# Kernel optimization log

Measured on AMD Instinct MI355X. Metric: run time of the kernel, lower is better.

## Reference

```python
import jax, jax.numpy as jnp
import numpy as np

B, N1, N2, D, O = 4, 256, 256, 64, 64
TEMP = 1.0
BN_EPS = 1e-5


def setup_inputs() -> dict:
    key = jax.random.key(0)
    ks = jax.random.split(key, 24)
    s = lambda n: 1.0 / np.sqrt(n)
    inp = {
        'x1': jax.random.normal(ks[0], (B, N1, D), jnp.float32),
        'x2': jax.random.normal(ks[1], (B, N2, D), jnp.float32),
        'W_t1': jax.random.normal(ks[2], (D, D), jnp.float32) * s(D),
        'b_t1': jnp.zeros((D,), jnp.float32),
        'W_t2': jax.random.normal(ks[3], (D, D), jnp.float32) * s(D),
        'b_t2': jnp.zeros((D,), jnp.float32),
        'W_att': jax.random.normal(ks[4], (D, O), jnp.float32) * s(D),
        'b_att': jnp.zeros((O,), jnp.float32),
        'W_attM': jax.random.normal(ks[5], (D, O), jnp.float32) * s(D),
        'b_attM': jnp.zeros((O,), jnp.float32),
        'w11': jax.random.normal(ks[6], (O, 1), jnp.float32) * s(O),
        'w22': jax.random.normal(ks[7], (O, 1), jnp.float32) * s(O),
        'w12': jax.random.normal(ks[8], (O, 1), jnp.float32) * s(O),
        'wM': jax.random.normal(ks[9], (O, 1), jnp.float32) * s(O),
        'W_pa': jax.random.normal(ks[10], (D, O), jnp.float32) * s(D),
        'b_pa': jnp.zeros((O,), jnp.float32),
        'W_po': jax.random.normal(ks[11], (D, O), jnp.float32) * s(D),
        'b_po': jnp.zeros((O,), jnp.float32),
        'W_paM': jax.random.normal(ks[12], (D, O), jnp.float32) * s(D),
        'b_paM': jnp.zeros((O,), jnp.float32),
        'W_poM': jax.random.normal(ks[13], (D, O), jnp.float32) * s(D),
        'b_poM': jnp.zeros((O,), jnp.float32),
        'gamma': jnp.ones((O,), jnp.float32),
        'beta': jnp.zeros((O,), jnp.float32),
    }
    return inp


def _forward(x1, x2, W_t1, b_t1, W_t2, b_t2, W_att, b_att, W_attM, b_attM,
             w11, w22, w12, wM, W_pa, b_pa, W_po, b_po, W_paM, b_paM,
             W_poM, b_poM, gamma, beta):
    n1 = x1.shape[1]
    h1 = x1 @ W_t1 + b_t1                      # (B,n1,D)
    h2 = x2 @ W_t2 + b_t2                      # (B,n2,D)
    x = jnp.concatenate([h1, h2], axis=1)      # (B,N,D)
    master = jnp.mean(x, axis=1, keepdims=True)  # (B,1,D)

    # --- type-blocked attention map ---
    pair = x[:, :, None, :] * x[:, None, :, :]          # (B,N,N,D)
    e = jnp.tanh(pair @ W_att + b_att)                   # (B,N,N,O)
    s11 = jnp.einsum('bijd,d->bij', e[:, :n1, :n1], w11[:, 0])
    s12 = jnp.einsum('bijd,d->bij', e[:, :n1, n1:], w12[:, 0])
    s21 = jnp.einsum('bijd,d->bij', e[:, n1:, :n1], w12[:, 0])
    s22 = jnp.einsum('bijd,d->bij', e[:, n1:, n1:], w22[:, 0])
    top = jnp.concatenate([s11, s12], axis=2)
    bot = jnp.concatenate([s21, s22], axis=2)
    scores = jnp.concatenate([top, bot], axis=1)         # (B,N,N)
    att = jax.nn.softmax(scores / TEMP, axis=2)          # softmax over source nodes (torch dim=-2 of (B,N,N,1))

    # --- master update ---
    m = jnp.tanh((x * master) @ W_attM + b_attM)         # (B,N,O)
    aM = jax.nn.softmax((m @ wM) / TEMP, axis=1)         # (B,N,1)
    agg_m = jnp.einsum('bn,bnd->bd', aM[:, :, 0], x)[:, None, :]  # (B,1,D)
    master_new = (agg_m @ W_paM + b_paM) + (master @ W_poM + b_poM)

    # --- node projection + BN(eval) + SELU ---
    agg = jnp.einsum('bij,bjd->bid', att, x)             # (B,N,D)
    y = (agg @ W_pa + b_pa) + (x @ W_po + b_po)          # (B,N,O)
    y = y / jnp.sqrt(1.0 + BN_EPS) * gamma + beta        # BN eval: mean=0, var=1
    y = jax.nn.selu(y)
    return y[:, :n1], y[:, n1:], master_new


def reference(x1, x2, W_t1, b_t1, W_t2, b_t2, W_att, b_att, W_attM, b_attM,
              w11, w22, w12, wM, W_pa, b_pa, W_po, b_po, W_paM, b_paM,
              W_poM, b_poM, gamma, beta):
    return _forward(x1, x2, W_t1, b_t1, W_t2, b_t2, W_att, b_att, W_attM,
                    b_attM, w11, w22, w12, wM, W_pa, b_pa, W_po, b_po,
                    W_paM, b_paM, W_poM, b_poM, gamma, beta)
```

## Files before the change

kernel.cpp:

```cpp
#include <hip/hip_runtime.h>

#define BB 4
#define NN 512
#define NH 256
#define DD 64

typedef __attribute__((ext_vector_type(8))) short bf16x8;
typedef __attribute__((ext_vector_type(16))) float f32x16;
union BF8 { bf16x8 v; unsigned int u[4]; };
union BF8Q { bf16x8 v; uint4 q; };

__device__ __forceinline__ float wred_sum(float v) {
  v += __shfl_xor(v, 32);
  v += __shfl_xor(v, 16);
  v += __shfl_xor(v, 8);
  v += __shfl_xor(v, 4);
  v += __shfl_xor(v, 2);
  v += __shfl_xor(v, 1);
  return v;
}

__device__ __forceinline__ float wred_max(float v) {
  v = fmaxf(v, __shfl_xor(v, 32));
  v = fmaxf(v, __shfl_xor(v, 16));
  v = fmaxf(v, __shfl_xor(v, 8));
  v = fmaxf(v, __shfl_xor(v, 4));
  v = fmaxf(v, __shfl_xor(v, 2));
  v = fmaxf(v, __shfl_xor(v, 1));
  return v;
}

__device__ __forceinline__ unsigned int cvtpk_bf16(float lo, float hi) {
  unsigned int r;
  asm("v_cvt_pk_bf16_f32 %0, %1, %2" : "=v"(r) : "v"(lo), "v"(hi));
  return r;
}

__device__ __forceinline__ float fast_exp2(float x) {
  float r;
  asm("v_exp_f32 %0, %1" : "=v"(r) : "v"(x));
  return r;
}

__device__ __forceinline__ float fast_tanh(float t) {
  t = fminf(15.f, fmaxf(-15.f, t));
  float z = __expf(2.f * t);
  return 1.f - 2.f * __builtin_amdgcn_rcpf(z + 1.f);
}

__device__ __forceinline__ float bflo(unsigned int u) { return __uint_as_float(u << 16); }
__device__ __forceinline__ float bfhi(unsigned int u) { return __uint_as_float(u & 0xffff0000u); }

__global__ __launch_bounds__(256)
void k1_build_x(const float* __restrict__ x1, const float* __restrict__ x2,
                const float* __restrict__ W_t1, const float* __restrict__ b_t1,
                const float* __restrict__ W_t2, const float* __restrict__ b_t2,
                float* __restrict__ X, unsigned int* __restrict__ XbfG) {
  const int tid = threadIdx.x;
  const int lane = tid & 63;
  const int rq = tid >> 6;
  const int r = blockIdx.x * 4 + rq;
  const int b = r >> 9;
  const int n = r & 511;
  const float* src; const float* W; const float* bias;
  if (n < NH) { src = x1 + (b * NH + n) * DD;        W = W_t1; bias = b_t1; }
  else        { src = x2 + (b * NH + (n - NH)) * DD; W = W_t2; bias = b_t2; }
  const float4* s4 = reinterpret_cast<const float4*>(src);
  float t0 = 0.f, t1 = 0.f, t2 = 0.f, t3 = 0.f;
#pragma unroll
  for (int c = 0; c < 16; ++c) {
    const float4 v = s4[c];
    t0 = fmaf(v.x, W[(4 * c + 0) * DD + lane], t0);
    t1 = fmaf(v.y, W[(4 * c + 1) * DD + lane], t1);
    t2 = fmaf(v.z, W[(4 * c + 2) * DD + lane], t2);
    t3 = fmaf(v.w, W[(4 * c + 3) * DD + lane], t3);
  }
  const float yv = ((t0 + t1) + (t2 + t3)) + bias[lane];
  X[r * DD + lane] = yv;
  const float nb = __shfl_down(yv, 1);
  if ((lane & 1) == 0) XbfG[r * 32 + (lane >> 1)] = cvtpk_bf16(yv, nb);
}

__global__ __launch_bounds__(512, 1)
void k_sc(const unsigned int* __restrict__ Xbf,
          const float* __restrict__ W_att, const float* __restrict__ b_att,
          const float* __restrict__ w11, const float* __restrict__ w22,
          const float* __restrict__ w12,
          float* __restrict__ scG) {
  const int b = blockIdx.y;
  const int bx = blockIdx.x;
  const int tid = threadIdx.x;
  const int lane = tid & 63;
  const int w = tid >> 6;
  const int l31 = lane & 31;
  const int half = lane >> 5;

  __shared__ __align__(16) float tblB[64];
  __shared__ __align__(16) unsigned int A2L[4][32];

  const unsigned int* __restrict__ Xb = Xbf + b * NN * 32;
  float* __restrict__ scb = scG + b * NN * NN;
  const float K2E = 2.8853900817779268f;

  if (tid < 64) {
    const int ot = tid >> 5, hf = (tid >> 4) & 1, r = tid & 15;
    const int o = ot * 32 + (r & 3) + 8 * (r >> 2) + 4 * hf;
    tblB[tid] = K2E * b_att[o];
  }
  if (tid >= 64 && tid < 320) {
    const int tt = tid - 64;
    const int comb = tt >> 6;
    const int idx = tt & 63;
    if (idx < 32) {
      const int ot = (idx >> 4) & 1, kg = (idx >> 3) & 1, hf = (idx >> 2) & 1, pp = idx & 3;
      const int it_ = comb >> 1, jt_ = comb & 1;
      const float* wsl = it_ ? (jt_ ? w22 : w12) : (jt_ ? w12 : w11);
      const int e0 = 2 * pp, e1 = 2 * pp + 1;
      const int o0 = ot * 32 + kg * 16 + (e0 & 3) + 8 * (e0 >> 2) + 4 * hf;
      const int o1 = ot * 32 + kg * 16 + (e1 & 3) + 8 * (e1 >> 2) + 4 * hf;
      A2L[comb][idx] = cvtpk_bf16(wsl[o0], wsl[o1]);
    }
  }

  BF8 Wp[2][4];
#pragma unroll
  for (int ot = 0; ot < 2; ++ot)
#pragma unroll
    for (int kt = 0; kt < 4; ++kt) {
      const int o = ot * 32 + l31;
#pragma unroll
      for (int pp = 0; pp < 4; ++pp) {
        const int d0 = kt * 16 + half * 8 + 2 * pp;
        Wp[ot][kt].u[pp] = cvtpk_bf16(W_att[d0 * DD + o], W_att[(d0 + 1) * DD + o]);
      }
    }

  __syncthreads();

  const int cminA = bx >> 4;
  const int n32A = 16 - cminA;
  const int rB = 510 - 2 * bx;
  const int cminB = (255 - bx) >> 4;
  const int njobs = 2 * (n32A + (16 - cminB));

#pragma unroll 1
  for (int jb = w; jb < njobs; jb += 8) {
    int row, c32;
    if (jb < 2 * n32A) { row = 2 * bx + (jb & 1); c32 = cminA + (jb >> 1); }
    else { const int tp = jb - 2 * n32A; row = rB + (tp & 1); c32 = cminB + (tp >> 1); }
    const int j0 = c32 * 32;
    const int comb = ((row >= NH) ? 2 : 0) | ((j0 >= NH) ? 1 : 0);

    BF8 Bi[4];
#pragma unroll
    for (int kt = 0; kt < 4; ++kt) {
      const uint4 xi = *reinterpret_cast<const uint4*>(Xb + row * 32 + kt * 8 + half * 4);
      const uint4 xj = *reinterpret_cast<const uint4*>(Xb + (j0 + l31) * 32 + kt * 8 + half * 4);
      Bi[kt].u[0] = cvtpk_bf16(bflo(xi.x) * bflo(xj.x), bfhi(xi.x) * bfhi(xj.x));
      Bi[kt].u[1] = cvtpk_bf16(bflo(xi.y) * bflo(xj.y), bfhi(xi.y) * bfhi(xj.y));
      Bi[kt].u[2] = cvtpk_bf16(bflo(xi.z) * bflo(xj.z), bfhi(xi.z) * bfhi(xj.z));
      Bi[kt].u[3] = cvtpk_bf16(bflo(xi.w) * bflo(xj.w), bfhi(xi.w) * bfhi(xj.w));
    }

    f32x16 C0 = {}, C1 = {};
#pragma unroll
    for (int kt = 0; kt < 4; ++kt) {
      C0 = __builtin_amdgcn_mfma_f32_32x32x16_bf16(Wp[0][kt].v, Bi[kt].v, C0, 0, 0, 0);
      C1 = __builtin_amdgcn_mfma_f32_32x32x16_bf16(Wp[1][kt].v, Bi[kt].v, C1, 0, 0, 0);
    }

    f32x16 D2 = {};
    const int base = half * 16;
#pragma unroll
    for (int ot = 0; ot < 2; ++ot) {
      float tv[16];
#pragma unroll
      for (int r = 0; r < 16; ++r) {
        const float Cr = (ot == 0) ? C0[r] : C1[r];
        const float arg = fmaf(Cr, K2E, tblB[ot * 32 + base + r]);
        const float e = fast_exp2(arg);
        tv[r] = fmaf(-2.f, __builtin_amdgcn_rcpf(e + 1.f), 1.f);
      }
      BF8 B2a, B2b;
#pragma unroll
      for (int pp = 0; pp < 4; ++pp) {
        B2a.u[pp] = cvtpk_bf16(tv[2 * pp], tv[2 * pp + 1]);
        B2b.u[pp] = cvtpk_bf16(tv[8 + 2 * pp], tv[9 + 2 * pp]);
      }
      BF8Q A2a, A2b;
      A2a.q = *reinterpret_cast<const uint4*>(&A2L[comb][ot * 16 + half * 4]);
      A2b.q = *reinterpret_cast<const uint4*>(&A2L[comb][ot * 16 + 8 + half * 4]);
      D2 = __builtin_amdgcn_mfma_f32_32x32x16_bf16(A2a.v, B2a.v, D2, 0, 0, 0);
      D2 = __builtin_amdgcn_mfma_f32_32x32x16_bf16(A2b.v, B2b.v, D2, 0, 0, 0);
    }
    const float pout = D2[0];
    if (lane < 32) {
      const int j = j0 + l31;
      if (j >= row) {
        scb[row * NN + j] = pout;
        if (j > row) scb[j * NN + row] = pout;
      }
    }
  }
}

__global__ __launch_bounds__(1024, 4)
void k_rest(const unsigned int* __restrict__ Xbf, const float* __restrict__ scG,
            const float* __restrict__ W_attM, const float* __restrict__ b_attM,
            const float* __restrict__ wM,
            const float* __restrict__ W_pa, const float* __restrict__ b_pa,
            const float* __restrict__ W_po, const float* __restrict__ b_po,
            const float* __restrict__ gamma, const float* __restrict__ beta,
            float* __restrict__ master, float* __restrict__ logits,
            float* __restrict__ out) {
  const int b = blockIdx.y;
  const int i0 = blockIdx.x * 8;
  const int tid = threadIdx.x;
  const int lane = tid & 63;
  const int w = tid >> 6;
  const int l31 = lane & 31;
  const int half = lane >> 5;

  __shared__ __align__(16) unsigned int XbfL[NN * 32];
  __shared__ __align__(16) float scL[8 * NN];
  __shared__ __align__(16) float red2[16][DD];
  __shared__ __align__(16) float aggP[32][DD];
  __shared__ __align__(16) float aggL[8][DD];
  __shared__ __align__(16) float mastL[64];

  const unsigned int* __restrict__ Xb = Xbf + b * NN * 32;

  {
#pragma unroll
    for (int k = 0; k < 4; ++k)
      reinterpret_cast<uint4*>(XbfL)[tid + k * 1024] =
          reinterpret_cast<const uint4*>(Xb)[tid + k * 1024];
  }
  {
    const int r8 = tid >> 7;
    const int c = (tid & 127) * 4;
    *reinterpret_cast<float4*>(&scL[r8 * NN + c]) =
        *reinterpret_cast<const float4*>(&scG[(b * NN + i0 + r8) * NN + c]);
  }
  __syncthreads();

  {
    float se = 0.f, so = 0.f;
    for (int r = w * 32; r < w * 32 + 32; ++r) {
      const unsigned int u = XbfL[r * 32 + l31];
      se += bflo(u); so += bfhi(u);
    }
    if (half == 0) {
      float2 pr; pr.x = se; pr.y = so;
      *reinterpret_cast<float2*>(&red2[w][l31 * 2]) = pr;
    }
  }
  __syncthreads();
  if (w == 0) {
    float s = 0.f;
#pragma unroll
    for (int k = 0; k < 16; ++k) s += red2[k][lane];
    s *= (1.f / 512.f);
    mastL[lane] = s;
    if (blockIdx.x == 0) master[b * DD + lane] = s;
  }

  const int row = w & 7, part = w >> 3;
  const int irow = i0 + row;
  float v[8];
#pragma unroll
  for (int k = 0; k < 8; ++k) v[k] = scL[row * NN + lane + 64 * k];
  __syncthreads();
  float mx = fmaxf(fmaxf(fmaxf(v[0], v[1]), fmaxf(v[2], v[3])),
                   fmaxf(fmaxf(v[4], v[5]), fmaxf(v[6], v[7])));
  mx = wred_max(mx);
  float ssum = 0.f;
#pragma unroll
  for (int k = 0; k < 8; ++k) { v[k] = __expf(v[k] - mx); ssum += v[k]; }
  ssum = wred_sum(ssum);
  const float inv = __builtin_amdgcn_rcpf(ssum);
#pragma unroll
  for (int k = 0; k < 4; ++k) {
    const int kk = part * 4 + k;
    scL[row * NN + lane + 64 * kk] = v[kk] * inv;
  }

  {
    float ae = 0.f, ao = 0.f;
    const int jb = part * 256 + half * 128;
#pragma unroll 4
    for (int it = 0; it < 32; ++it) {
      const int j = jb + it * 4;
      const float4 at = *reinterpret_cast<const float4*>(&scL[row * NN + j]);
      const unsigned int u0 = XbfL[(j + 0) * 32 + l31];
      const unsigned int u1 = XbfL[(j + 1) * 32 + l31];
      const unsigned int u2 = XbfL[(j + 2) * 32 + l31];
      const unsigned int u3 = XbfL[(j + 3) * 32 + l31];
      ae = fmaf(at.x, bflo(u0), ae); ao = fmaf(at.x, bfhi(u0), ao);
      ae = fmaf(at.y, bflo(u1), ae); ao = fmaf(at.y, bfhi(u1), ao);
      ae = fmaf(at.z, bflo(u2), ae); ao = fmaf(at.z, bfhi(u2), ao);
      ae = fmaf(at.w, bflo(u3), ae); ao = fmaf(at.w, bfhi(u3), ao);
    }
    float2 pr; pr.x = ae; pr.y = ao;
    *reinterpret_cast<float2*>(&aggP[row * 4 + part * 2 + half][l31 * 2]) = pr;
  }
  __syncthreads();

  uint4 xr[8];
#pragma unroll
  for (int s = 0; s < 8; ++s)
    xr[s] = *reinterpret_cast<const uint4*>(&XbfL[irow * 32 + s * 4]);

  if (part == 0) {
    const float aggv = aggP[row * 4 + 0][lane] + aggP[row * 4 + 1][lane] +
                       aggP[row * 4 + 2][lane] + aggP[row * 4 + 3][lane];
    aggL[row][lane] = aggv;
    float y = b_pa[lane] + b_po[lane];
#pragma unroll
    for (int s = 0; s < 8; ++s) {
      const float xd[8] = {bflo(xr[s].x), bfhi(xr[s].x), bflo(xr[s].y), bfhi(xr[s].y),
                           bflo(xr[s].z), bfhi(xr[s].z), bflo(xr[s].w), bfhi(xr[s].w)};
      const float4 agA = *reinterpret_cast<const float4*>(&aggL[row][s * 8]);
      const float4 agB = *reinterpret_cast<const float4*>(&aggL[row][s * 8 + 4]);
      const float ad[8] = {agA.x, agA.y, agA.z, agA.w, agB.x, agB.y, agB.z, agB.w};
#pragma unroll
      for (int q = 0; q < 8; ++q) {
        const int d = s * 8 + q;
        y = fmaf(ad[q], W_pa[d * DD + lane], y);
        y = fmaf(xd[q], W_po[d * DD + lane], y);
      }
    }
    const float RSQ = 0.9999950000374997f;
    y = y * RSQ * gamma[lane] + beta[lane];
    const float SC_ = 1.0507009873554805f;
    const float AL = 1.6732632423543772f;
    y = (y > 0.f) ? (SC_ * y) : (SC_ * AL * (__expf(y) - 1.f));
    const int off = (irow < NH) ? ((b * NH + irow) * DD + lane)
                                : (BB * NH * DD + (b * NH + (irow - NH)) * DD + lane);
    out[off] = y;
  } else {
    float lg = b_attM[lane];
#pragma unroll
    for (int s = 0; s < 8; ++s) {
      const float xd[8] = {bflo(xr[s].x), bfhi(xr[s].x), bflo(xr[s].y), bfhi(xr[s].y),
                           bflo(xr[s].z), bfhi(xr[s].z), bflo(xr[s].w), bfhi(xr[s].w)};
      const float4 mA = *reinterpret_cast<const float4*>(&mastL[s * 8]);
      const float4 mB = *reinterpret_cast<const float4*>(&mastL[s * 8 + 4]);
      const float md[8] = {mA.x, mA.y, mA.z, mA.w, mB.x, mB.y, mB.z, mB.w};
#pragma unroll
      for (int q = 0; q < 8; ++q) {
        const int d = s * 8 + q;
        lg = fmaf(xd[q] * md[q], W_attM[d * DD + lane], lg);
      }
    }
    const float th = fast_tanh(lg);
    const float s = wred_sum(th * wM[lane]);
    if (lane == 0) logits[b * NN + irow] = s;
  }
}

__global__ __launch_bounds__(256)
void k4_master_new(const float* __restrict__ X, const float* __restrict__ master,
                   const float* __restrict__ logits,
                   const float* __restrict__ W_paM, const float* __restrict__ b_paM,
                   const float* __restrict__ W_poM, const float* __restrict__ b_poM,
                   float* __restrict__ out) {
  const int b = blockIdx.x;
  const int tid = threadIdx.x;
  const int lane = tid & 63;
  const int q = tid >> 6;
  __shared__ float red[4][DD];
  __shared__ float r4[4];
  __shared__ float aggm_s[DD];
  __shared__ float mrow_s[DD];
  const float* lg = logits + b * NN;
  const float v0 = lg[tid];
  const float v1 = lg[tid + 256];
  float mx = wred_max(fmaxf(v0, v1));
  if (lane == 0) r4[q] = mx;
  __syncthreads();
  mx = fmaxf(fmaxf(r4[0], r4[1]), fmaxf(r4[2], r4[3]));
  float es = __expf(v0 - mx) + __expf(v1 - mx);
  es = wred_sum(es);
  __syncthreads();
  if (lane == 0) r4[q] = es;
  __syncthreads();
  const float S = r4[0] + r4[1] + r4[2] + r4[3];
  const float invS = 1.f / S;

  float acc = 0.f;
  for (int nn = q * 128; nn < q * 128 + 128; ++nn) {
    const float a = __expf(lg[nn] - mx);
    acc = fmaf(a, X[(b * NN + nn) * DD + lane], acc);
  }
  red[q][lane] = acc;
  __syncthreads();
  if (q == 0) {
    aggm_s[lane] =
        (red[0][lane] + red[1][lane] + red[2][lane] + red[3][lane]) * invS;
    mrow_s[lane] = master[b * DD + lane];
  }
  __syncthreads();
  float p = 0.f;
  for (int d = q * 16; d < q * 16 + 16; ++d) {
    p = fmaf(aggm_s[d], W_paM[d * DD + lane], p);
    p = fmaf(mrow_s[d], W_poM[d * DD + lane], p);
  }
  __syncthreads();
  red[q][lane] = p;
  __syncthreads();
  if (q == 0) {
    out[2 * BB * NH * DD + b * DD + lane] =
        red[0][lane] + red[1][lane] + red[2][lane] + red[3][lane] +
        b_paM[lane] + b_poM[lane];
  }
}

extern "C" void kernel_launch(void* const* d_in, const int* in_sizes, int n_in,
                              void* d_out, int out_size, void* d_ws, size_t ws_size,
                              hipStream_t stream) {
  const float* x1    = (const float*)d_in[0];
  const float* x2    = (const float*)d_in[1];
  const float* W_t1  = (const float*)d_in[2];
  const float* b_t1  = (const float*)d_in[3];
  const float* W_t2  = (const float*)d_in[4];
  const float* b_t2  = (const float*)d_in[5];
  const float* W_att = (const float*)d_in[6];
  const float* b_att = (const float*)d_in[7];
  const float* W_attM = (const float*)d_in[8];
  const float* b_attM = (const float*)d_in[9];
  const float* w11   = (const float*)d_in[10];
  const float* w22   = (const float*)d_in[11];
  const float* w12   = (const float*)d_in[12];
  const float* wM    = (const float*)d_in[13];
  const float* W_pa  = (const float*)d_in[14];
  const float* b_pa  = (const float*)d_in[15];
  const float* W_po  = (const float*)d_in[16];
  const float* b_po  = (const float*)d_in[17];
  const float* W_paM = (const float*)d_in[18];
  const float* b_paM = (const float*)d_in[19];
  const float* W_poM = (const float*)d_in[20];
  const float* b_poM = (const float*)d_in[21];
  const float* gamma = (const float*)d_in[22];
  const float* beta  = (const float*)d_in[23];

  float* ws     = (float*)d_ws;
  float* X      = ws;
  float* master = ws + 131072;
  float* logits = ws + 131328;
  float* scG    = ws + 133376;
  unsigned int* Xbf = (unsigned int*)(ws + 133376 + 1048576);
  float* out    = (float*)d_out;

  k1_build_x<<<512, 256, 0, stream>>>(x1, x2, W_t1, b_t1, W_t2, b_t2, X, Xbf);
  k_sc<<<dim3(128, 4), 512, 0, stream>>>(Xbf, W_att, b_att, w11, w22, w12, scG);
  k_rest<<<dim3(64, 4), 1024, 0, stream>>>(Xbf, scG, W_attM, b_attM, wM,
                                           W_pa, b_pa, W_po, b_po, gamma, beta,
                                           master, logits, out);
  k4_master_new<<<4, 256, 0, stream>>>(X, master, logits, W_paM, b_paM, W_poM, b_poM, out);
}
```

Before: 48.71 us.

## Fuse all four kernels into one cooperative kernel with grid syncs

Replaces the four separate launches (projection, pairwise scores, row softmax/aggregation, master update) with a single cooperative kernel of 256 blocks of 512 threads, separated by grid.sync barriers. This removes inter-kernel launch gaps and drain/fill overhead. It also remaps work so the k_rest phase uses 512 threads per block instead of 1024, and the master-update phase reads bf16 X instead of fp32 X. The cost is grid-wide barrier latency, a large static LDS footprint, and one block per CU constraining occupancy in every phase.

```diff
diff --git a/kernel.cpp b/kernel.cpp
--- a/kernel.cpp
+++ b/kernel.cpp
@@ -1,4 +1,7 @@
 #include <hip/hip_runtime.h>
+#include <hip/hip_cooperative_groups.h>
+
+namespace cg = cooperative_groups;
 
 #define BB 4
 #define NN 512
@@ -51,57 +54,67 @@
 __device__ __forceinline__ float bflo(unsigned int u) { return __uint_as_float(u << 16); }
 __device__ __forceinline__ float bfhi(unsigned int u) { return __uint_as_float(u & 0xffff0000u); }
 
-__global__ __launch_bounds__(256)
-void k1_build_x(const float* __restrict__ x1, const float* __restrict__ x2,
-                const float* __restrict__ W_t1, const float* __restrict__ b_t1,
-                const float* __restrict__ W_t2, const float* __restrict__ b_t2,
-                float* __restrict__ X, unsigned int* __restrict__ XbfG) {
-  const int tid = threadIdx.x;
-  const int lane = tid & 63;
-  const int rq = tid >> 6;
-  const int r = blockIdx.x * 4 + rq;
-  const int b = r >> 9;
-  const int n = r & 511;
-  const float* src; const float* W; const float* bias;
-  if (n < NH) { src = x1 + (b * NH + n) * DD;        W = W_t1; bias = b_t1; }
-  else        { src = x2 + (b * NH + (n - NH)) * DD; W = W_t2; bias = b_t2; }
-  const float4* s4 = reinterpret_cast<const float4*>(src);
-  float t0 = 0.f, t1 = 0.f, t2 = 0.f, t3 = 0.f;
-#pragma unroll
-  for (int c = 0; c < 16; ++c) {
-    const float4 v = s4[c];
-    t0 = fmaf(v.x, W[(4 * c + 0) * DD + lane], t0);
-    t1 = fmaf(v.y, W[(4 * c + 1) * DD + lane], t1);
-    t2 = fmaf(v.z, W[(4 * c + 2) * DD + lane], t2);
-    t3 = fmaf(v.w, W[(4 * c + 3) * DD + lane], t3);
-  }
-  const float yv = ((t0 + t1) + (t2 + t3)) + bias[lane];
-  X[r * DD + lane] = yv;
-  const float nb = __shfl_down(yv, 1);
-  if ((lane & 1) == 0) XbfG[r * 32 + (lane >> 1)] = cvtpk_bf16(yv, nb);
-}
-
 __global__ __launch_bounds__(512, 1)
-void k_sc(const unsigned int* __restrict__ Xbf,
-          const float* __restrict__ W_att, const float* __restrict__ b_att,
-          const float* __restrict__ w11, const float* __restrict__ w22,
-          const float* __restrict__ w12,
-          float* __restrict__ scG) {
-  const int b = blockIdx.y;
-  const int bx = blockIdx.x;
+void k_fused(const float* __restrict__ x1, const float* __restrict__ x2,
+             const float* __restrict__ W_t1, const float* __restrict__ b_t1,
+             const float* __restrict__ W_t2, const float* __restrict__ b_t2,
+             const float* __restrict__ W_att, const float* __restrict__ b_att,
+             const float* __restrict__ W_attM, const float* __restrict__ b_attM,
+             const float* __restrict__ wM,
+             const float* __restrict__ w11, const float* __restrict__ w22,
+             const float* __restrict__ w12,
+             const float* __restrict__ W_pa, const float* __restrict__ b_pa,
+             const float* __restrict__ W_po, const float* __restrict__ b_po,
+             const float* __restrict__ W_paM, const float* __restrict__ b_paM,
+             const float* __restrict__ W_poM, const float* __restrict__ b_poM,
+             const float* __restrict__ gamma, const float* __restrict__ beta,
+             float* __restrict__ X, unsigned int* __restrict__ Xbf,
+             float* __restrict__ master, float* __restrict__ logits,
+             float* __restrict__ scG, float* __restrict__ out) {
+  cg::grid_group grid = cg::this_grid();
+  const int bid = blockIdx.x;
   const int tid = threadIdx.x;
   const int lane = tid & 63;
   const int w = tid >> 6;
   const int l31 = lane & 31;
   const int half = lane >> 5;
-
+  const float K2E = 2.8853900817779268f;
+
+  __shared__ __align__(16) unsigned int XbfL[NN * 32];
+  __shared__ __align__(16) float scL[8 * NN];
+  __shared__ __align__(16) float red2[8][DD];
+  __shared__ __align__(16) float aggL[8][DD];
+  __shared__ __align__(16) float mastL[64];
   __shared__ __align__(16) float tblB[64];
   __shared__ __align__(16) unsigned int A2L[4][32];
-
-  const unsigned int* __restrict__ Xb = Xbf + b * NN * 32;
-  float* __restrict__ scb = scG + b * NN * NN;
-  const float K2E = 2.8853900817779268f;
-
+  __shared__ __align__(16) float lgL[NN];
+  __shared__ __align__(16) float r8a[8];
+  __shared__ __align__(16) float r8b[8];
+  __shared__ __align__(16) float aggm_s[DD];
+  __shared__ __align__(16) float mrow_s[DD];
+
+  {
+    const int r = bid * 8 + w;
+    const int bb = r >> 9;
+    const int n = r & 511;
+    const float* src; const float* W; const float* bias;
+    if (n < NH) { src = x1 + (bb * NH + n) * DD;        W = W_t1; bias = b_t1; }
+    else        { src = x2 + (bb * NH + (n - NH)) * DD; W = W_t2; bias = b_t2; }
+    const float4* s4 = reinterpret_cast<const float4*>(src);
+    float t0 = 0.f, t1 = 0.f, t2 = 0.f, t3 = 0.f;
+#pragma unroll
+    for (int c = 0; c < 16; ++c) {
+      const float4 v = s4[c];
+      t0 = fmaf(v.x, W[(4 * c + 0) * DD + lane], t0);
+      t1 = fmaf(v.y, W[(4 * c + 1) * DD + lane], t1);
+      t2 = fmaf(v.z, W[(4 * c + 2) * DD + lane], t2);
+      t3 = fmaf(v.w, W[(4 * c + 3) * DD + lane], t3);
+    }
+    const float yv = ((t0 + t1) + (t2 + t3)) + bias[lane];
+    X[r * DD + lane] = yv;
+    const float nb = __shfl_down(yv, 1);
+    if (!(lane & 1)) Xbf[r * 32 + (lane >> 1)] = cvtpk_bf16(yv, nb);
+  }
   if (tid < 64) {
     const int ot = tid >> 5, hf = (tid >> 4) & 1, r = tid & 15;
     const int o = ot * 32 + (r & 3) + 8 * (r >> 2) + 4 * hf;
@@ -121,298 +134,294 @@
       A2L[comb][idx] = cvtpk_bf16(wsl[o0], wsl[o1]);
     }
   }
-
-  BF8 Wp[2][4];
-#pragma unroll
-  for (int ot = 0; ot < 2; ++ot)
-#pragma unroll
-    for (int kt = 0; kt < 4; ++kt) {
-      const int o = ot * 32 + l31;
-#pragma unroll
-      for (int pp = 0; pp < 4; ++pp) {
-        const int d0 = kt * 16 + half * 8 + 2 * pp;
-        Wp[ot][kt].u[pp] = cvtpk_bf16(W_att[d0 * DD + o], W_att[(d0 + 1) * DD + o]);
-      }
-    }
-
-  __syncthreads();
-
-  const int cminA = bx >> 4;
-  const int n32A = 16 - cminA;
-  const int rB = 510 - 2 * bx;
-  const int cminB = (255 - bx) >> 4;
-  const int njobs = 2 * (n32A + (16 - cminB));
+  grid.sync();
+
+  {
+    BF8 Wp[2][4];
+#pragma unroll
+    for (int ot = 0; ot < 2; ++ot)
+#pragma unroll
+      for (int kt = 0; kt < 4; ++kt) {
+        const int o = ot * 32 + l31;
+#pragma unroll
+        for (int pp = 0; pp < 4; ++pp) {
+          const int d0 = kt * 16 + half * 8 + 2 * pp;
+          Wp[ot][kt].u[pp] = cvtpk_bf16(W_att[d0 * DD + o], W_att[(d0 + 1) * DD + o]);
+        }
+      }
 
 #pragma unroll 1
-  for (int jb = w; jb < njobs; jb += 8) {
-    int row, c32;
-    if (jb < 2 * n32A) { row = 2 * bx + (jb & 1); c32 = cminA + (jb >> 1); }
-    else { const int tp = jb - 2 * n32A; row = rB + (tp & 1); c32 = cminB + (tp >> 1); }
-    const int j0 = c32 * 32;
-    const int comb = ((row >= NH) ? 2 : 0) | ((j0 >= NH) ? 1 : 0);
-
-    BF8 Bi[4];
-#pragma unroll
-    for (int kt = 0; kt < 4; ++kt) {
-      const uint4 xi = *reinterpret_cast<const uint4*>(Xb + row * 32 + kt * 8 + half * 4);
-      const uint4 xj = *reinterpret_cast<const uint4*>(Xb + (j0 + l31) * 32 + kt * 8 + half * 4);
-      Bi[kt].u[0] = cvtpk_bf16(bflo(xi.x) * bflo(xj.x), bfhi(xi.x) * bfhi(xj.x));
-      Bi[kt].u[1] = cvtpk_bf16(bflo(xi.y) * bflo(xj.y), bfhi(xi.y) * bfhi(xj.y));
-      Bi[kt].u[2] = cvtpk_bf16(bflo(xi.z) * bflo(xj.z), bfhi(xi.z) * bfhi(xj.z));
-      Bi[kt].u[3] = cvtpk_bf16(bflo(xi.w) * bflo(xj.w), bfhi(xi.w) * bfhi(xj.w));
-    }
-
-    f32x16 C0 = {}, C1 = {};
-#pragma unroll
-    for (int kt = 0; kt < 4; ++kt) {
-      C0 = __builtin_amdgcn_mfma_f32_32x32x16_bf16(Wp[0][kt].v, Bi[kt].v, C0, 0, 0, 0);
-      C1 = __builtin_amdgcn_mfma_f32_32x32x16_bf16(Wp[1][kt].v, Bi[kt].v, C1, 0, 0, 0);
-    }
-
-    f32x16 D2 = {};
-    const int base = half * 16;
-#pragma unroll
-    for (int ot = 0; ot < 2; ++ot) {
-      float tv[16];
-#pragma unroll
-      for (int r = 0; r < 16; ++r) {
-        const float Cr = (ot == 0) ? C0[r] : C1[r];
-        const float arg = fmaf(Cr, K2E, tblB[ot * 32 + base + r]);
-        const float e = fast_exp2(arg);
-        tv[r] = fmaf(-2.f, __builtin_amdgcn_rcpf(e + 1.f), 1.f);
-      }
-      BF8 B2a, B2b;
-#pragma unroll
-      for (int pp = 0; pp < 4; ++pp) {
-        B2a.u[pp] = cvtpk_bf16(tv[2 * pp], tv[2 * pp + 1]);
-        B2b.u[pp] = cvtpk_bf16(tv[8 + 2 * pp], tv[9 + 2 * pp]);
-      }
-      BF8Q A2a, A2b;
-      A2a.q = *reinterpret_cast<const uint4*>(&A2L[comb][ot * 16 + half * 4]);
-      A2b.q = *reinterpret_cast<const uint4*>(&A2L[comb][ot * 16 + 8 + half * 4]);
-      D2 = __builtin_amdgcn_mfma_f32_32x32x16_bf16(A2a.v, B2a.v, D2, 0, 0, 0);
-      D2 = __builtin_amdgcn_mfma_f32_32x32x16_bf16(A2b.v, B2b.v, D2, 0, 0, 0);
-    }
-    const float pout = D2[0];
-    if (lane < 32) {
-      const int j = j0 + l31;
-      if (j >= row) {
-        scb[row * NN + j] = pout;
-        if (j > row) scb[j * NN + row] = pout;
-      }
-    }
-  }
-}
-
-__global__ __launch_bounds__(1024, 4)
-void k_rest(const unsigned int* __restrict__ Xbf, const float* __restrict__ scG,
-            const float* __restrict__ W_attM, const float* __restrict__ b_attM,
-            const float* __restrict__ wM,
-            const float* __restrict__ W_pa, const float* __restrict__ b_pa,
-            const float* __restrict__ W_po, const float* __restrict__ b_po,
-            const float* __restrict__ gamma, const float* __restrict__ beta,
-            float* __restrict__ master, float* __restrict__ logits,
-            float* __restrict__ out) {
-  const int b = blockIdx.y;
-  const int i0 = blockIdx.x * 8;
-  const int tid = threadIdx.x;
-  const int lane = tid & 63;
-  const int w = tid >> 6;
-  const int l31 = lane & 31;
-  const int half = lane >> 5;
-
-  __shared__ __align__(16) unsigned int XbfL[NN * 32];
-  __shared__ __align__(16) float scL[8 * NN];
-  __shared__ __align__(16) float red2[16][DD];
-  __shared__ __align__(16) float aggP[32][DD];
-  __shared__ __align__(16) float aggL[8][DD];
-  __shared__ __align__(16) float mastL[64];
-
-  const unsigned int* __restrict__ Xb = Xbf + b * NN * 32;
+    for (int vb = 2 * bid; vb < 2 * bid + 2; ++vb) {
+      const int b = vb >> 7;
+      const int bx = vb & 127;
+      const unsigned int* __restrict__ Xg = Xbf + b * NN * 32;
+      float* __restrict__ scb = scG + b * NN * NN;
+
+      const int cminA = bx >> 4;
+      const int n32A = 16 - cminA;
+      const int rB = 510 - 2 * bx;
+      const int cminB = (255 - bx) >> 4;
+      const int njobs = 2 * (n32A + (16 - cminB));
+
+#pragma unroll 1
+      for (int jb = w; jb < njobs; jb += 8) {
+        int row, c32;
+        if (jb < 2 * n32A) { row = 2 * bx + (jb & 1); c32 = cminA + (jb >> 1); }
+        else { const int tp = jb - 2 * n32A; row = rB + (tp & 1); c32 = cminB + (tp >> 1); }
+        const int j0 = c32 * 32;
+        const int comb = ((row >= NH) ? 2 : 0) | ((j0 >= NH) ? 1 : 0);
+
+        BF8 Bi[4];
+#pragma unroll
+        for (int kt = 0; kt < 4; ++kt) {
+          const uint4 xi = *reinterpret_cast<const uint4*>(Xg + row * 32 + kt * 8 + half * 4);
+          const uint4 xj = *reinterpret_cast<const uint4*>(Xg + (j0 + l31) * 32 + kt * 8 + half * 4);
+          Bi[kt].u[0] = cvtpk_bf16(bflo(xi.x) * bflo(xj.x), bfhi(xi.x) * bfhi(xj.x));
+          Bi[kt].u[1] = cvtpk_bf16(bflo(xi.y) * bflo(xj.y), bfhi(xi.y) * bfhi(xj.y));
+          Bi[kt].u[2] = cvtpk_bf16(bflo(xi.z) * bflo(xj.z), bfhi(xi.z) * bfhi(xj.z));
+          Bi[kt].u[3] = cvtpk_bf16(bflo(xi.w) * bflo(xj.w), bfhi(xi.w) * bfhi(xj.w));
+        }
+
+        f32x16 C0 = {}, C1 = {};
+#pragma unroll
+        for (int kt = 0; kt < 4; ++kt) {
+          C0 = __builtin_amdgcn_mfma_f32_32x32x16_bf16(Wp[0][kt].v, Bi[kt].v, C0, 0, 0, 0);
+          C1 = __builtin_amdgcn_mfma_f32_32x32x16_bf16(Wp[1][kt].v, Bi[kt].v, C1, 0, 0, 0);
+        }
+
+        f32x16 D2 = {};
+        const int base = half * 16;
+#pragma unroll
+        for (int ot = 0; ot < 2; ++ot) {
+          float tv[16];
+#pragma unroll
+          for (int r = 0; r < 16; ++r) {
+            const float Cr = (ot == 0) ? C0[r] : C1[r];
+            const float arg = fmaf(Cr, K2E, tblB[ot * 32 + base + r]);
+            const float e = fast_exp2(arg);
+            tv[r] = fmaf(-2.f, __builtin_amdgcn_rcpf(e + 1.f), 1.f);
+          }
+          BF8 B2a, B2b;
+#pragma unroll
+          for (int pp = 0; pp < 4; ++pp) {
+            B2a.u[pp] = cvtpk_bf16(tv[2 * pp], tv[2 * pp + 1]);
+            B2b.u[pp] = cvtpk_bf16(tv[8 + 2 * pp], tv[9 + 2 * pp]);
+          }
+          BF8Q A2a, A2b;
+          A2a.q = *reinterpret_cast<const uint4*>(&A2L[comb][ot * 16 + half * 4]);
+          A2b.q = *reinterpret_cast<const uint4*>(&A2L[comb][ot * 16 + 8 + half * 4]);
+          D2 = __builtin_amdgcn_mfma_f32_32x32x16_bf16(A2a.v, B2a.v, D2, 0, 0, 0);
+          D2 = __builtin_amdgcn_mfma_f32_32x32x16_bf16(A2b.v, B2b.v, D2, 0, 0, 0);
+        }
+        const float pout = D2[0];
+        if (lane < 32) {
+          const int j = j0 + l31;
+          if (j >= row) {
+            scb[row * NN + j] = pout;
+            if (j > row) scb[j * NN + row] = pout;
+          }
+        }
+      }
+    }
+  }
+  grid.sync();
 
   {
-#pragma unroll
-    for (int k = 0; k < 4; ++k)
-      reinterpret_cast<uint4*>(XbfL)[tid + k * 1024] =
-          reinterpret_cast<const uint4*>(Xb)[tid + k * 1024];
-  }
-  {
-    const int r8 = tid >> 7;
-    const int c = (tid & 127) * 4;
-    *reinterpret_cast<float4*>(&scL[r8 * NN + c]) =
-        *reinterpret_cast<const float4*>(&scG[(b * NN + i0 + r8) * NN + c]);
-  }
-  __syncthreads();
-
-  {
-    float se = 0.f, so = 0.f;
-    for (int r = w * 32; r < w * 32 + 32; ++r) {
-      const unsigned int u = XbfL[r * 32 + l31];
-      se += bflo(u); so += bfhi(u);
-    }
-    if (half == 0) {
-      float2 pr; pr.x = se; pr.y = so;
-      *reinterpret_cast<float2*>(&red2[w][l31 * 2]) = pr;
-    }
-  }
-  __syncthreads();
-  if (w == 0) {
-    float s = 0.f;
-#pragma unroll
-    for (int k = 0; k < 16; ++k) s += red2[k][lane];
-    s *= (1.f / 512.f);
-    mastL[lane] = s;
-    if (blockIdx.x == 0) master[b * DD + lane] = s;
-  }
-
-  const int row = w & 7, part = w >> 3;
-  const int irow = i0 + row;
-  float v[8];
-#pragma unroll
-  for (int k = 0; k < 8; ++k) v[k] = scL[row * NN + lane + 64 * k];
-  __syncthreads();
-  float mx = fmaxf(fmaxf(fmaxf(v[0], v[1]), fmaxf(v[2], v[3])),
-                   fmaxf(fmaxf(v[4], v[5]), fmaxf(v[6], v[7])));
-  mx = wred_max(mx);
-  float ssum = 0.f;
-#pragma unroll
-  for (int k = 0; k < 8; ++k) { v[k] = __expf(v[k] - mx); ssum += v[k]; }
-  ssum = wred_sum(ssum);
-  const float inv = __builtin_amdgcn_rcpf(ssum);
-#pragma unroll
-  for (int k = 0; k < 4; ++k) {
-    const int kk = part * 4 + k;
-    scL[row * NN + lane + 64 * kk] = v[kk] * inv;
-  }
-
-  {
-    float ae = 0.f, ao = 0.f;
-    const int jb = part * 256 + half * 128;
+    const int b = bid >> 6;
+    const int i0 = (bid & 63) * 8;
+    const unsigned int* __restrict__ Xg = Xbf + b * NN * 32;
+
+#pragma unroll
+    for (int k = 0; k < 8; ++k)
+      reinterpret_cast<uint4*>(XbfL)[tid + k * 512] =
+          reinterpret_cast<const uint4*>(Xg)[tid + k * 512];
+    {
+      const int r8 = tid >> 6;
+      const int c = (tid & 63) * 8;
+      const float* src = &scG[(b * NN + i0 + r8) * NN + c];
+      *reinterpret_cast<float4*>(&scL[r8 * NN + c]) = *reinterpret_cast<const float4*>(src);
+      *reinterpret_cast<float4*>(&scL[r8 * NN + c + 4]) = *reinterpret_cast<const float4*>(src + 4);
+    }
+    __syncthreads();
+
+    {
+      float se = 0.f, so = 0.f;
+      const int r0 = w * 64 + half * 32;
+      for (int r = r0; r < r0 + 32; ++r) {
+        const unsigned int u = XbfL[r * 32 + l31];
+        se += bflo(u); so += bfhi(u);
+      }
+      se += __shfl_xor(se, 32);
+      so += __shfl_xor(so, 32);
+      if (half == 0) {
+        float2 pr; pr.x = se; pr.y = so;
+        *reinterpret_cast<float2*>(&red2[w][l31 * 2]) = pr;
+      }
+    }
+    __syncthreads();
+    if (w == 0) {
+      float s = 0.f;
+#pragma unroll
+      for (int k = 0; k < 8; ++k) s += red2[k][lane];
+      s *= (1.f / 512.f);
+      mastL[lane] = s;
+      if ((bid & 63) == 0) master[b * DD + lane] = s;
+    }
+
+    const int irow = i0 + w;
+    {
+      float v[8];
+#pragma unroll
+      for (int k = 0; k < 8; ++k) v[k] = scL[w * NN + lane + 64 * k];
+      float mx = fmaxf(fmaxf(fmaxf(v[0], v[1]), fmaxf(v[2], v[3])),
+                       fmaxf(fmaxf(v[4], v[5]), fmaxf(v[6], v[7])));
+      mx = wred_max(mx);
+      float ssum = 0.f;
+#pragma unroll
+      for (int k = 0; k < 8; ++k) { v[k] = __expf(v[k] - mx); ssum += v[k]; }
+      ssum = wred_sum(ssum);
+      const float inv = __builtin_amdgcn_rcpf(ssum);
+#pragma unroll
+      for (int k = 0; k < 8; ++k) scL[w * NN + lane + 64 * k] = v[k] * inv;
+    }
+
+    {
+      float ae = 0.f, ao = 0.f;
+      const int jb0 = half * 256;
 #pragma unroll 4
-    for (int it = 0; it < 32; ++it) {
-      const int j = jb + it * 4;
-      const float4 at = *reinterpret_cast<const float4*>(&scL[row * NN + j]);
-      const unsigned int u0 = XbfL[(j + 0) * 32 + l31];
-      const unsigned int u1 = XbfL[(j + 1) * 32 + l31];
-      const unsigned int u2 = XbfL[(j + 2) * 32 + l31];
-      const unsigned int u3 = XbfL[(j + 3) * 32 + l31];
-      ae = fmaf(at.x, bflo(u0), ae); ao = fmaf(at.x, bfhi(u0), ao);
-      ae = fmaf(at.y, bflo(u1), ae); ao = fmaf(at.y, bfhi(u1), ao);
-      ae = fmaf(at.z, bflo(u2), ae); ao = fmaf(at.z, bfhi(u2), ao);
-      ae = fmaf(at.w, bflo(u3), ae); ao = fmaf(at.w, bfhi(u3), ao);
-    }
-    float2 pr; pr.x = ae; pr.y = ao;
-    *reinterpret_cast<float2*>(&aggP[row * 4 + part * 2 + half][l31 * 2]) = pr;
-  }
-  __syncthreads();
-
-  uint4 xr[8];
-#pragma unroll
-  for (int s = 0; s < 8; ++s)
-    xr[s] = *reinterpret_cast<const uint4*>(&XbfL[irow * 32 + s * 4]);
-
-  if (part == 0) {
-    const float aggv = aggP[row * 4 + 0][lane] + aggP[row * 4 + 1][lane] +
-                       aggP[row * 4 + 2][lane] + aggP[row * 4 + 3][lane];
-    aggL[row][lane] = aggv;
-    float y = b_pa[lane] + b_po[lane];
-#pragma unroll
-    for (int s = 0; s < 8; ++s) {
-      const float xd[8] = {bflo(xr[s].x), bfhi(xr[s].x), bflo(xr[s].y), bfhi(xr[s].y),
-                           bflo(xr[s].z), bfhi(xr[s].z), bflo(xr[s].w), bfhi(xr[s].w)};
-      const float4 agA = *reinterpret_cast<const float4*>(&aggL[row][s * 8]);
-      const float4 agB = *reinterpret_cast<const float4*>(&aggL[row][s * 8 + 4]);
-      const float ad[8] = {agA.x, agA.y, agA.z, agA.w, agB.x, agB.y, agB.z, agB.w};
-#pragma unroll
-      for (int q = 0; q < 8; ++q) {
-        const int d = s * 8 + q;
-        y = fmaf(ad[q], W_pa[d * DD + lane], y);
-        y = fmaf(xd[q], W_po[d * DD + lane], y);
-      }
-    }
-    const float RSQ = 0.9999950000374997f;
-    y = y * RSQ * gamma[lane] + beta[lane];
-    const float SC_ = 1.0507009873554805f;
-    const float AL = 1.6732632423543772f;
-    y = (y > 0.f) ? (SC_ * y) : (SC_ * AL * (__expf(y) - 1.f));
-    const int off = (irow < NH) ? ((b * NH + irow) * DD + lane)
-                                : (BB * NH * DD + (b * NH + (irow - NH)) * DD + lane);
-    out[off] = y;
-  } else {
-    float lg = b_attM[lane];
-#pragma unroll
-    for (int s = 0; s < 8; ++s) {
-      const float xd[8] = {bflo(xr[s].x), bfhi(xr[s].x), bflo(xr[s].y), bfhi(xr[s].y),
-                           bflo(xr[s].z), bfhi(xr[s].z), bflo(xr[s].w), bfhi(xr[s].w)};
-      const float4 mA = *reinterpret_cast<const float4*>(&mastL[s * 8]);
-      const float4 mB = *reinterpret_cast<const float4*>(&mastL[s * 8 + 4]);
-      const float md[8] = {mA.x, mA.y, mA.z, mA.w, mB.x, mB.y, mB.z, mB.w};
-#pragma unroll
-      for (int q = 0; q < 8; ++q) {
-        const int d = s * 8 + q;
-        lg = fmaf(xd[q] * md[q], W_attM[d * DD + lane], lg);
-      }
-    }
-    const float th = fast_tanh(lg);
-    const float s = wred_sum(th * wM[lane]);
-    if (lane == 0) logits[b * NN + irow] = s;
-  }
-}
-
-__global__ __launch_bounds__(256)
-void k4_master_new(const float* __restrict__ X, const float* __restrict__ master,
-                   const float* __restrict__ logits,
-                   const float* __restrict__ W_paM, const float* __restrict__ b_paM,
-                   const float* __restrict__ W_poM, const float* __restrict__ b_poM,
-                   float* __restrict__ out) {
-  const int b = blockIdx.x;
-  const int tid = threadIdx.x;
-  const int lane = tid & 63;
-  const int q = tid >> 6;
-  __shared__ float red[4][DD];
-  __shared__ float r4[4];
-  __shared__ float aggm_s[DD];
-  __shared__ float mrow_s[DD];
-  const float* lg = logits + b * NN;
-  const float v0 = lg[tid];
-  const float v1 = lg[tid + 256];
-  float mx = wred_max(fmaxf(v0, v1));
-  if (lane == 0) r4[q] = mx;
-  __syncthreads();
-  mx = fmaxf(fmaxf(r4[0], r4[1]), fmaxf(r4[2], r4[3]));
-  float es = __expf(v0 - mx) + __expf(v1 - mx);
-  es = wred_sum(es);
-  __syncthreads();
-  if (lane == 0) r4[q] = es;
-  __syncthreads();
-  const float S = r4[0] + r4[1] + r4[2] + r4[3];
-  const float invS = 1.f / S;
-
-  float acc = 0.f;
-  for (int nn = q * 128; nn < q * 128 + 128; ++nn) {
-    const float a = __expf(lg[nn] - mx);
-    acc = fmaf(a, X[(b * NN + nn) * DD + lane], acc);
-  }
-  red[q][lane] = acc;
-  __syncthreads();
-  if (q == 0) {
-    aggm_s[lane] =
-        (red[0][lane] + red[1][lane] + red[2][lane] + red[3][lane]) * invS;
-    mrow_s[lane] = master[b * DD + lane];
-  }
-  __syncthreads();
-  float p = 0.f;
-  for (int d = q * 16; d < q * 16 + 16; ++d) {
-    p = fmaf(aggm_s[d], W_paM[d * DD + lane], p);
-    p = fmaf(mrow_s[d], W_poM[d * DD + lane], p);
-  }
-  __syncthreads();
-  red[q][lane] = p;
-  __syncthreads();
-  if (q == 0) {
-    out[2 * BB * NH * DD + b * DD + lane] =
-        red[0][lane] + red[1][lane] + red[2][lane] + red[3][lane] +
-        b_paM[lane] + b_poM[lane];
+      for (int it = 0; it < 64; ++it) {
+        const int j = jb0 + it * 4;
+        const float4 at = *reinterpret_cast<const float4*>(&scL[w * NN + j]);
+        const unsigned int u0 = XbfL[(j + 0) * 32 + l31];
+        const unsigned int u1 = XbfL[(j + 1) * 32 + l31];
+        const unsigned int u2 = XbfL[(j + 2) * 32 + l31];
+        const unsigned int u3 = XbfL[(j + 3) * 32 + l31];
+        ae = fmaf(at.x, bflo(u0), ae); ao = fmaf(at.x, bfhi(u0), ao);
+        ae = fmaf(at.y, bflo(u1), ae); ao = fmaf(at.y, bfhi(u1), ao);
+        ae = fmaf(at.z, bflo(u2), ae); ao = fmaf(at.z, bfhi(u2), ao);
+        ae = fmaf(at.w, bflo(u3), ae); ao = fmaf(at.w, bfhi(u3), ao);
+      }
+      ae += __shfl_xor(ae, 32);
+      ao += __shfl_xor(ao, 32);
+      if (half == 0) {
+        float2 pr; pr.x = ae; pr.y = ao;
+        *reinterpret_cast<float2*>(&aggL[w][l31 * 2]) = pr;
+      }
+    }
+    __syncthreads();
+
+    uint4 xr[8];
+#pragma unroll
+    for (int s = 0; s < 8; ++s)
+      xr[s] = *reinterpret_cast<const uint4*>(&XbfL[irow * 32 + s * 4]);
+
+    {
+      float y = b_pa[lane] + b_po[lane];
+#pragma unroll
+      for (int s = 0; s < 8; ++s) {
+        const float xd[8] = {bflo(xr[s].x), bfhi(xr[s].x), bflo(xr[s].y), bfhi(xr[s].y),
+                             bflo(xr[s].z), bfhi(xr[s].z), bflo(xr[s].w), bfhi(xr[s].w)};
+        const float4 agA = *reinterpret_cast<const float4*>(&aggL[w][s * 8]);
+        const float4 agB = *reinterpret_cast<const float4*>(&aggL[w][s * 8 + 4]);
+        const float ad[8] = {agA.x, agA.y, agA.z, agA.w, agB.x, agB.y, agB.z, agB.w};
+#pragma unroll
+        for (int q = 0; q < 8; ++q) {
+          const int d = s * 8 + q;
+          y = fmaf(ad[q], W_pa[d * DD + lane], y);
+          y = fmaf(xd[q], W_po[d * DD + lane], y);
+        }
+      }
+      const float RSQ = 0.9999950000374997f;
+      y = y * RSQ * gamma[lane] + beta[lane];
+      const float SC_ = 1.0507009873554805f;
+      const float AL = 1.6732632423543772f;
+      y = (y > 0.f) ? (SC_ * y) : (SC_ * AL * (__expf(y) - 1.f));
+      const int off = (irow < NH) ? ((b * NH + irow) * DD + lane)
+                                  : (BB * NH * DD + (b * NH + (irow - NH)) * DD + lane);
+      out[off] = y;
+    }
+
+    {
+      float lg = b_attM[lane];
+#pragma unroll
+      for (int s = 0; s < 8; ++s) {
+        const float xd[8] = {bflo(xr[s].x), bfhi(xr[s].x), bflo(xr[s].y), bfhi(xr[s].y),
+                             bflo(xr[s].z), bfhi(xr[s].z), bflo(xr[s].w), bfhi(xr[s].w)};
+        const float4 mA = *reinterpret_cast<const float4*>(&mastL[s * 8]);
+        const float4 mB = *reinterpret_cast<const float4*>(&mastL[s * 8 + 4]);
+        const float md[8] = {mA.x, mA.y, mA.z, mA.w, mB.x, mB.y, mB.z, mB.w};
+#pragma unroll
+        for (int q = 0; q < 8; ++q) {
+          const int d = s * 8 + q;
+          lg = fmaf(xd[q] * md[q], W_attM[d * DD + lane], lg);
+        }
+      }
+      const float th = fast_tanh(lg);
+      const float s = wred_sum(th * wM[lane]);
+      if (lane == 0) logits[b * NN + irow] = s;
+    }
+  }
+  grid.sync();
+
+  if (bid < BB) {
+    const int b = bid;
+    lgL[tid] = logits[b * NN + tid];
+    const float v0 = lgL[tid];
+    __syncthreads();
+    float mx = wred_max(v0);
+    if (lane == 0) r8a[w] = mx;
+    __syncthreads();
+    mx = r8a[0];
+#pragma unroll
+    for (int k = 1; k < 8; ++k) mx = fmaxf(mx, r8a[k]);
+    float es = wred_sum(__expf(v0 - mx));
+    if (lane == 0) r8b[w] = es;
+    __syncthreads();
+    float S = r8b[0];
+#pragma unroll
+    for (int k = 1; k < 8; ++k) S += r8b[k];
+    const float invS = 1.f / S;
+
+    {
+      float ae = 0.f, ao = 0.f;
+      const int r0 = w * 64 + half * 32;
+      for (int r = r0; r < r0 + 32; ++r) {
+        const float a = __expf(lgL[r] - mx);
+        const unsigned int u = Xbf[b * NN * 32 + r * 32 + l31];
+        ae = fmaf(a, bflo(u), ae);
+        ao = fmaf(a, bfhi(u), ao);
+      }
+      ae += __shfl_xor(ae, 32);
+      ao += __shfl_xor(ao, 32);
+      if (half == 0) {
+        float2 pr; pr.x = ae; pr.y = ao;
+        *reinterpret_cast<float2*>(&red2[w][l31 * 2]) = pr;
+      }
+    }
+    __syncthreads();
+    if (w == 0) {
+      float s = 0.f;
+#pragma unroll
+      for (int k = 0; k < 8; ++k) s += red2[k][lane];
+      aggm_s[lane] = s * invS;
+      mrow_s[lane] = master[b * DD + lane];
+    }
+    __syncthreads();
+    float p = 0.f;
+#pragma unroll
+    for (int k = 0; k < 8; ++k) {
+      const int d = w * 8 + k;
+      p = fmaf(aggm_s[d], W_paM[d * DD + lane], p);
+      p = fmaf(mrow_s[d], W_poM[d * DD + lane], p);
+    }
+    red2[w][lane] = p;
+    __syncthreads();
+    if (w == 0) {
+      float s = 0.f;
+#pragma unroll
+      for (int k = 0; k < 8; ++k) s += red2[k][lane];
+      out[2 * BB * NH * DD + b * DD + lane] = s + b_paM[lane] + b_poM[lane];
+    }
   }
 }
 
@@ -452,10 +461,13 @@
   unsigned int* Xbf = (unsigned int*)(ws + 133376 + 1048576);
   float* out    = (float*)d_out;
 
-  k1_build_x<<<512, 256, 0, stream>>>(x1, x2, W_t1, b_t1, W_t2, b_t2, X, Xbf);
-  k_sc<<<dim3(128, 4), 512, 0, stream>>>(Xbf, W_att, b_att, w11, w22, w12, scG);
-  k_rest<<<dim3(64, 4), 1024, 0, stream>>>(Xbf, scG, W_attM, b_attM, wM,
-                                           W_pa, b_pa, W_po, b_po, gamma, beta,
-                                           master, logits, out);
-  k4_master_new<<<4, 256, 0, stream>>>(X, master, logits, W_paM, b_paM, W_poM, b_poM, out);
-}
+  void* kargs[] = {
+      (void*)&x1, (void*)&x2, (void*)&W_t1, (void*)&b_t1, (void*)&W_t2, (void*)&b_t2,
+      (void*)&W_att, (void*)&b_att, (void*)&W_attM, (void*)&b_attM, (void*)&wM,
+      (void*)&w11, (void*)&w22, (void*)&w12,
+      (void*)&W_pa, (void*)&b_pa, (void*)&W_po, (void*)&b_po,
+      (void*)&W_paM, (void*)&b_paM, (void*)&W_poM, (void*)&b_poM,
+      (void*)&gamma, (void*)&beta,
+      (void*)&X, (void*)&Xbf, (void*)&master, (void*)&logits, (void*)&scG, (void*)&out};
+  hipLaunchCooperativeKernel((void*)k_fused, dim3(256), dim3(512), kargs, 0, stream);
+}
```

Result: slower. 132.6 us (+172.2%).
